# Performance work log

Hardware: AMD Instinct MI355X
Metric: run time of the kernel (lower is better)

The kernel has to match this reference:

```python
import jax, jax.numpy as jnp
import numpy as np

I, H, O = 512, 1024, 2  # input_size, hidden_size, output_size
B, S = 64, 512          # batch, seq_len


def setup_inputs() -> dict:
    key = jax.random.key(0)
    ks = jax.random.split(key, 9)
    sc = 1.0 / np.sqrt(I + H)
    return {
        "x": jax.random.normal(ks[0], (B, S, I), dtype=jnp.float32),
        "h": jnp.zeros((B, 1, H), dtype=jnp.float32),
        "Wz": jax.random.uniform(ks[1], (I + H, H), jnp.float32, -sc, sc),
        "bz": jax.random.uniform(ks[2], (H,), jnp.float32, -sc, sc),
        "Wr": jax.random.uniform(ks[3], (I + H, H), jnp.float32, -sc, sc),
        "br": jax.random.uniform(ks[4], (H,), jnp.float32, -sc, sc),
        "Wh": jax.random.uniform(ks[5], (I + H, H), jnp.float32, -sc, sc),
        "bh": jax.random.uniform(ks[6], (H,), jnp.float32, -sc, sc),
        "Wfc": jax.random.uniform(ks[7], (H, O), jnp.float32, -1.0 / np.sqrt(H), 1.0 / np.sqrt(H)),
        "bfc": jax.random.uniform(ks[8], (O,), jnp.float32, -1.0 / np.sqrt(H), 1.0 / np.sqrt(H)),
    }


def reference(x, h, Wz, bz, Wr, br, Wh, bh, Wfc, bfc):
    h0 = jnp.squeeze(h, axis=1)  # (B, H)

    def step(hid, xt):  # xt: (B, I), hid: (B, H)
        ih = jnp.concatenate([xt, hid], axis=1)              # (B, I+H)
        z = jax.nn.sigmoid(ih @ Wz + bz)                     # update gate
        r = jax.nn.sigmoid(ih @ Wr + br)                     # reset gate
        ihr = jnp.concatenate([xt, r * hid], axis=1)
        h_cand = jnp.tanh(ihr @ Wh + bh)
        new_h = (1.0 - z) * hid + z * h_cand
        return new_h, None

    x_t = jnp.transpose(x, (1, 0, 2))  # (S, B, I)
    h_last, _ = jax.lax.scan(step, h0, x_t)
    out = jax.nn.relu(h_last) @ Wfc + bfc  # (B, O)
    return jax.nn.log_softmax(out, axis=1)
```

## Files before the change

### kernel.cpp

```cpp
#include <hip/hip_runtime.h>

typedef __attribute__((ext_vector_type(4))) short bf4;
typedef __attribute__((ext_vector_type(8))) short bf8;
typedef __attribute__((ext_vector_type(4))) float f4;

#define BB 64
#define SS 512
#define II 512
#define HH 1024
#define SCH 64
#define NCH 8
#define GBLK 64

__device__ __forceinline__ short f2bf(float f) {
  unsigned u = __float_as_uint(f);
  u = u + 0x7fff + ((u >> 16) & 1);
  return (short)(u >> 16);
}
__device__ __forceinline__ float bf2f(short s) {
  return __uint_as_float(((unsigned)(unsigned short)s) << 16);
}
__device__ __forceinline__ float sigm(float x) {
  return 1.0f / (1.0f + __expf(-x));
}
__device__ __forceinline__ float tanh_f(float x) {
  float e = __expf(-2.0f * fabsf(x));
  float t = (1.0f - e) / (1.0f + e);
  return copysignf(t, x);
}

__device__ __forceinline__ unsigned long long ld_u64_l3(const unsigned long long* p) {
  return __hip_atomic_load((unsigned long long*)p, __ATOMIC_RELAXED, __HIP_MEMORY_SCOPE_AGENT);
}
__device__ __forceinline__ void st_u32_l3(unsigned* p, unsigned v) {
  __hip_atomic_store(p, v, __ATOMIC_RELAXED, __HIP_MEMORY_SCOPE_AGENT);
}


__global__ __launch_bounds__(256) void cast_x_k(const float* __restrict__ x, short* __restrict__ xb) {
  size_t i = ((size_t)blockIdx.x * 256 + threadIdx.x) * 4;
  float4 v = *(const float4*)(x + i);
  bf4 o; o[0] = f2bf(v.x); o[1] = f2bf(v.y); o[2] = f2bf(v.z); o[3] = f2bf(v.w);
  *(bf4*)(xb + i) = o;
}

__global__ __launch_bounds__(256) void prep_wxt_k(const float* __restrict__ Wz, const float* __restrict__ Wr,
                                                  const float* __restrict__ Wh, short* __restrict__ WxT) {
  int idx = blockIdx.x * 256 + threadIdx.x;
  int g = idx >> 19;
  int rem = idx & 524287;
  int n = rem >> 9, k = rem & 511;
  const float* W = (g == 0) ? Wz : (g == 1) ? Wr : Wh;
  WxT[idx] = f2bf(W[(size_t)k * HH + n]);
}

__global__ __launch_bounds__(256) void prep_uswz_k(const float* __restrict__ Wz, const float* __restrict__ Wr,
                                                   const float* __restrict__ Wh, short* __restrict__ Us) {
  int t = blockIdx.x * 256 + threadIdx.x;
  int lane = t & 63, kk = (t >> 6) & 31, nb = (t >> 11) & 63, g = t >> 17;
  const float* W = (g == 0) ? Wz : (g == 1) ? Wr : Wh;
  int n = nb * 16 + (lane & 15);
  int kb = II + kk * 32 + (lane >> 4) * 8;
  bf8 o;
#pragma unroll
  for (int j = 0; j < 8; j++) o[j] = f2bf(W[(size_t)(kb + j) * HH + n]);
  *(bf8*)(Us + (size_t)t * 8) = o;
}

__global__ __launch_bounds__(256) void init_h_k(const float* __restrict__ h, float* __restrict__ h32,
                                                short* __restrict__ hb) {
  int i = blockIdx.x * 256 + threadIdx.x;
  float v = h[i];
  h32[i] = v; hb[i] = f2bf(v);
}

__global__ __launch_bounds__(256) void gemm_k(const short* __restrict__ xb, const short* __restrict__ WxT,
                                              const float* __restrict__ bz, const float* __restrict__ br,
                                              const float* __restrict__ bh, short* __restrict__ Gx, int s0) {
  __shared__ short Al[4 * 64 * 8];
  __shared__ short Bl[4 * 64 * 8];
  int tid = threadIdx.x, wave = tid >> 6, lane = tid & 63;
  int sl = blockIdx.x;
  int n0 = blockIdx.y * 64;
  f4 acc[4] = {};
  int mp = tid >> 2, q = tid & 3;
  const short* asrc = xb + ((size_t)mp * SS + (s0 + sl)) * II + q * 8;
  int ng = n0 + mp;
  int gb = ng >> 10, hb_ = ng & 1023;
  const short* bsrc = WxT + ((size_t)gb * HH + hb_) * II + q * 8;
  int adst = ((mp >> 4) * 64 + q * 16 + (mp & 15)) * 8;

  for (int kk = 0; kk < II; kk += 32) {
    bf8 av = *(const bf8*)(asrc + kk);
    bf8 bv = *(const bf8*)(bsrc + kk);
    __syncthreads();
    *(bf8*)&Al[adst] = av;
    *(bf8*)&Bl[adst] = bv;
    __syncthreads();
    bf8 af = *(bf8*)&Al[(wave * 64 + lane) * 8];
#pragma unroll
    for (int ns = 0; ns < 4; ns++) {
      bf8 bfr = *(bf8*)&Bl[(ns * 64 + lane) * 8];
      acc[ns] = __builtin_amdgcn_mfma_f32_16x16x32_bf16(af, bfr, acc[ns], 0, 0, 0);
    }
  }
  int brow0 = wave * 16 + (lane >> 4) * 4;
#pragma unroll
  for (int ns = 0; ns < 4; ns++) {
    int ngl = n0 + ns * 16 + (lane & 15);
    int g2 = ngl >> 10, h2 = ngl & 1023;
    float bias = ((g2 == 0) ? bz : (g2 == 1) ? br : bh)[h2];
    bf4 o;
#pragma unroll
    for (int i = 0; i < 4; i++) o[i] = f2bf(acc[ns][i] + bias);
    *(bf4*)&Gx[(((size_t)sl * 3 + g2) * HH + h2) * BB + brow0] = o;
  }
}


__device__ __forceinline__ void gbar(unsigned* flags, unsigned target) {
  __syncthreads();
  if (threadIdx.x == 0)
    __hip_atomic_store(&flags[blockIdx.x], target, __ATOMIC_RELEASE, __HIP_MEMORY_SCOPE_AGENT);
  if (threadIdx.x < GBLK) {
    while (__hip_atomic_load(&flags[threadIdx.x], __ATOMIC_RELAXED, __HIP_MEMORY_SCOPE_AGENT) < target)
      __builtin_amdgcn_s_sleep(1);
  }
  __asm__ volatile("" ::: "memory");
  __syncthreads();
}

union HL { unsigned long long u[2]; bf8 v; };

__global__ __launch_bounds__(256) void rec_k(const short* __restrict__ Gx, const short* __restrict__ Us,
                                             float* __restrict__ h32, short* hb,
                                             short* rhb, unsigned* flags) {
  __shared__ short Uzr[2 * 32 * 64 * 8];
  int tid = threadIdx.x, wave = tid >> 6, lane = tid & 63, bid = blockIdx.x;
  {
    const bf8* sz = (const bf8*)Us + ((size_t)(0 * 64 + bid)) * 2048;
    const bf8* sr = (const bf8*)Us + ((size_t)(1 * 64 + bid)) * 2048;
    bf8* d = (bf8*)Uzr;
    for (int i = tid; i < 2048; i += 256) { d[i] = sz[i]; d[2048 + i] = sr[i]; }
  }
  const bf8* Uh = (const bf8*)Us + ((size_t)(2 * 64 + bid)) * 2048;

  int n0 = bid * 16;
  int brow0 = wave * 16 + (lane >> 4) * 4;
  int ncol = n0 + (lane & 15);
  float hreg[4];
#pragma unroll
  for (int i = 0; i < 4; i++) hreg[i] = h32[(size_t)(brow0 + i) * HH + ncol];
  __syncthreads();

  size_t aoff = ((size_t)(wave * 16 + (lane & 15)) * HH + (lane >> 4) * 8) / 4;
  const unsigned long long* hq  = (const unsigned long long*)hb  + aoff;
  const unsigned long long* rhq = (const unsigned long long*)rhb + aoff;

  unsigned target = 0;
  for (int t = 0; t < SCH; t++) {
    const short* gz = Gx + (((size_t)t * 3 + 0) * HH + ncol) * BB + brow0;
    bf4 gzv = *(const bf4*)gz;
    bf4 grv = *(const bf4*)(gz + (size_t)HH * BB);
    bf4 ghv = *(const bf4*)(gz + 2 * (size_t)HH * BB);
    f4 zacc = {}, racc = {};
#pragma unroll
    for (int g = 0; g < 4; g++) {
      HL a[8];
#pragma unroll
      for (int j = 0; j < 8; j++) {
        int kk = g * 8 + j;
        a[j].u[0] = ld_u64_l3(hq + kk * 8);
        a[j].u[1] = ld_u64_l3(hq + kk * 8 + 1);
      }
#pragma unroll
      for (int j = 0; j < 8; j++) {
        int kk = g * 8 + j;
        bf8 b0 = *(bf8*)&Uzr[(kk * 64 + lane) * 8];
        zacc = __builtin_amdgcn_mfma_f32_16x16x32_bf16(a[j].v, b0, zacc, 0, 0, 0);
        bf8 b1 = *(bf8*)&Uzr[(2048 + kk * 64 + lane) * 8];
        racc = __builtin_amdgcn_mfma_f32_16x16x32_bf16(a[j].v, b1, racc, 0, 0, 0);
      }
    }
    float zf[4];
#pragma unroll
    for (int i = 0; i < 4; i++) {
      zf[i] = sigm(zacc[i] + bf2f(gzv[i]));
      float r = sigm(racc[i] + bf2f(grv[i]));
      unsigned sv = (unsigned)(unsigned short)f2bf(r * hreg[i]);
      unsigned up = __shfl_down(sv, 1);
      if (!(lane & 1))
        st_u32_l3((unsigned*)rhb + ((size_t)(brow0 + i) * HH + ncol) / 2, sv | (up << 16));
    }
    gbar(flags, ++target);
    f4 cacc = {};
#pragma unroll
    for (int g = 0; g < 4; g++) {
      HL a[8];
#pragma unroll
      for (int j = 0; j < 8; j++) {
        int kk = g * 8 + j;
        a[j].u[0] = ld_u64_l3(rhq + kk * 8);
        a[j].u[1] = ld_u64_l3(rhq + kk * 8 + 1);
      }
#pragma unroll
      for (int j = 0; j < 8; j++) {
        int kk = g * 8 + j;
        bf8 b2 = Uh[kk * 64 + lane];
        cacc = __builtin_amdgcn_mfma_f32_16x16x32_bf16(a[j].v, b2, cacc, 0, 0, 0);
      }
    }
#pragma unroll
    for (int i = 0; i < 4; i++) {
      float c = tanh_f(cacc[i] + bf2f(ghv[i]));
      float hn = hreg[i] + zf[i] * (c - hreg[i]);
      hreg[i] = hn;
      unsigned sv = (unsigned)(unsigned short)f2bf(hn);
      unsigned up = __shfl_down(sv, 1);
      if (!(lane & 1))
        st_u32_l3((unsigned*)hb + ((size_t)(brow0 + i) * HH + ncol) / 2, sv | (up << 16));
    }
    gbar(flags, ++target);
  }
#pragma unroll
  for (int i = 0; i < 4; i++) h32[(size_t)(brow0 + i) * HH + ncol] = hreg[i];
}


__global__ __launch_bounds__(64) void out_k(const float* __restrict__ h32, const float* __restrict__ Wfc,
                                            const float* __restrict__ bfc, float* __restrict__ out) {
  int b = blockIdx.x, t = threadIdx.x;
  float a0 = 0.f, a1 = 0.f;
  for (int k = t; k < HH; k += 64) {
    float hv = fmaxf(h32[(size_t)b * HH + k], 0.f);
    a0 += hv * Wfc[k * 2]; a1 += hv * Wfc[k * 2 + 1];
  }
#pragma unroll
  for (int off = 32; off > 0; off >>= 1) { a0 += __shfl_down(a0, off); a1 += __shfl_down(a1, off); }
  if (t == 0) {
    float y0 = a0 + bfc[0], y1 = a1 + bfc[1];
    float m = fmaxf(y0, y1);
    float lse = m + logf(__expf(y0 - m) + __expf(y1 - m));
    out[b * 2] = y0 - lse; out[b * 2 + 1] = y1 - lse;
  }
}


extern "C" void kernel_launch(void* const* d_in, const int* in_sizes, int n_in,
                              void* d_out, int out_size, void* d_ws, size_t ws_size,
                              hipStream_t stream) {
  const float* x   = (const float*)d_in[0];
  const float* h0  = (const float*)d_in[1];
  const float* Wz  = (const float*)d_in[2];
  const float* bz  = (const float*)d_in[3];
  const float* Wr  = (const float*)d_in[4];
  const float* br  = (const float*)d_in[5];
  const float* Wh  = (const float*)d_in[6];
  const float* bh  = (const float*)d_in[7];
  const float* Wfc = (const float*)d_in[8];
  const float* bfc = (const float*)d_in[9];
  float* out = (float*)d_out;

  char* ws = (char*)d_ws;
  short*    xb    = (short*)(ws);
  short*    WxT   = (short*)(ws + 33554432);
  short*    Us    = (short*)(ws + 36700160);
  short*    Gx    = (short*)(ws + 42991616);
  float*    h32   = (float*)(ws + 68157440);
  short*    hbuf  = (short*)(ws + 68419584);
  short*    rhb   = (short*)(ws + 68550656);
  unsigned* flags = (unsigned*)(ws + 68681728);

  cast_x_k<<<16384, 256, 0, stream>>>(x, xb);
  prep_wxt_k<<<6144, 256, 0, stream>>>(Wz, Wr, Wh, WxT);
  prep_uswz_k<<<1536, 256, 0, stream>>>(Wz, Wr, Wh, Us);
  init_h_k<<<256, 256, 0, stream>>>(h0, h32, hbuf);

  for (int c = 0; c < NCH; c++) {
    gemm_k<<<dim3(SCH, 48), 256, 0, stream>>>(xb, WxT, bz, br, bh, Gx, c * SCH);
    hipMemsetAsync(flags, 0, GBLK * sizeof(unsigned), stream);
    rec_k<<<GBLK, 256, 0, stream>>>(Gx, Us, h32, hbuf, rhb, flags);
  }
  out_k<<<BB, 64, 0, stream>>>(h32, Wfc, bfc, out);
}
```

Measured before the change: 11.65 ms.

## Replace flat grid barrier with hierarchical per-XCC counter barrier

```diff
diff --git a/kernel.cpp b/kernel.cpp
--- a/kernel.cpp
+++ b/kernel.cpp
@@ -12,6 +12,11 @@
 #define NCH 8
 #define GBLK 64
 
+#define F_GINIT 0
+#define F_XCNT  32
+#define F_XARR  320
+#define F_XFLAG 608
+
 __device__ __forceinline__ short f2bf(float f) {
   unsigned u = __float_as_uint(f);
   u = u + 0x7fff + ((u >> 16) & 1);
@@ -34,6 +39,12 @@
 }
 __device__ __forceinline__ void st_u32_l3(unsigned* p, unsigned v) {
   __hip_atomic_store(p, v, __ATOMIC_RELAXED, __HIP_MEMORY_SCOPE_AGENT);
+}
+__device__ __forceinline__ unsigned rmw_read(unsigned* p) {
+  return __hip_atomic_fetch_add(p, 0u, __ATOMIC_RELAXED, __HIP_MEMORY_SCOPE_AGENT);
+}
+__device__ __forceinline__ unsigned rmw_add1(unsigned* p) {
+  return __hip_atomic_fetch_add(p, 1u, __ATOMIC_RELAXED, __HIP_MEMORY_SCOPE_AGENT);
 }
 
 
@@ -118,18 +129,6 @@
 }
 
 
-__device__ __forceinline__ void gbar(unsigned* flags, unsigned target) {
-  __syncthreads();
-  if (threadIdx.x == 0)
-    __hip_atomic_store(&flags[blockIdx.x], target, __ATOMIC_RELEASE, __HIP_MEMORY_SCOPE_AGENT);
-  if (threadIdx.x < GBLK) {
-    while (__hip_atomic_load(&flags[threadIdx.x], __ATOMIC_RELAXED, __HIP_MEMORY_SCOPE_AGENT) < target)
-      __builtin_amdgcn_s_sleep(1);
-  }
-  __asm__ volatile("" ::: "memory");
-  __syncthreads();
-}
-
 union HL { unsigned long long u[2]; bf8 v; };
 
 __global__ __launch_bounds__(256) void rec_k(const short* __restrict__ Gx, const short* __restrict__ Us,
@@ -137,6 +136,16 @@
                                              short* rhb, unsigned* flags) {
   __shared__ short Uzr[2 * 32 * 64 * 8];
   int tid = threadIdx.x, wave = tid >> 6, lane = tid & 63, bid = blockIdx.x;
+
+  unsigned myxcc;
+  __asm__ volatile("s_getreg_b32 %0, hwreg(HW_REG_XCC_ID)" : "=s"(myxcc));
+  myxcc &= 7;
+
+  if (tid == 0) {
+    rmw_add1(&flags[F_XCNT + 32 * myxcc]);
+    rmw_add1(&flags[F_GINIT]);
+  }
+
   {
     const bf8* sz = (const bf8*)Us + ((size_t)(0 * 64 + bid)) * 2048;
     const bf8* sr = (const bf8*)Us + ((size_t)(1 * 64 + bid)) * 2048;
@@ -151,6 +160,13 @@
   float hreg[4];
 #pragma unroll
   for (int i = 0; i < 4; i++) hreg[i] = h32[(size_t)(brow0 + i) * HH + ncol];
+
+  unsigned pres = 0, nown = 0;
+  if (tid < 8) {
+    while (rmw_read(&flags[F_GINIT]) < GBLK) __builtin_amdgcn_s_sleep(2);
+    pres = rmw_read(&flags[F_XCNT + 32 * tid]);
+    if (tid == 0) nown = rmw_read(&flags[F_XCNT + 32 * myxcc]);
+  }
   __syncthreads();
 
   size_t aoff = ((size_t)(wave * 16 + (lane & 15)) * HH + (lane >> 4) * 8) / 4;
@@ -192,7 +208,20 @@
       if (!(lane & 1))
         st_u32_l3((unsigned*)rhb + ((size_t)(brow0 + i) * HH + ncol) / 2, sv | (up << 16));
     }
-    gbar(flags, ++target);
+    ++target;
+    __syncthreads();
+    if (tid == 0) {
+      unsigned old = rmw_add1(&flags[F_XARR + 32 * myxcc]);
+      if (old + 1 == nown * target) {
+        __asm__ volatile("buffer_wbl2 sc1" ::: "memory");
+        __asm__ volatile("s_waitcnt vmcnt(0)" ::: "memory");
+        rmw_add1(&flags[F_XFLAG + 32 * myxcc]);
+      }
+    }
+    if (tid < 8 && pres)
+      while (rmw_read(&flags[F_XFLAG + 32 * tid]) < target) __builtin_amdgcn_s_sleep(2);
+    __asm__ volatile("" ::: "memory");
+    __syncthreads();
     f4 cacc = {};
 #pragma unroll
     for (int g = 0; g < 4; g++) {
@@ -220,7 +249,20 @@
       if (!(lane & 1))
         st_u32_l3((unsigned*)hb + ((size_t)(brow0 + i) * HH + ncol) / 2, sv | (up << 16));
     }
-    gbar(flags, ++target);
+    ++target;
+    __syncthreads();
+    if (tid == 0) {
+      unsigned old = rmw_add1(&flags[F_XARR + 32 * myxcc]);
+      if (old + 1 == nown * target) {
+        __asm__ volatile("buffer_wbl2 sc1" ::: "memory");
+        __asm__ volatile("s_waitcnt vmcnt(0)" ::: "memory");
+        rmw_add1(&flags[F_XFLAG + 32 * myxcc]);
+      }
+    }
+    if (tid < 8 && pres)
+      while (rmw_read(&flags[F_XFLAG + 32 * tid]) < target) __builtin_amdgcn_s_sleep(2);
+    __asm__ volatile("" ::: "memory");
+    __syncthreads();
   }
 #pragma unroll
   for (int i = 0; i < 4; i++) h32[(size_t)(brow0 + i) * HH + ncol] = hreg[i];
@@ -278,7 +320,7 @@
 
   for (int c = 0; c < NCH; c++) {
     gemm_k<<<dim3(SCH, 48), 256, 0, stream>>>(xb, WxT, bz, br, bh, Gx, c * SCH);
-    hipMemsetAsync(flags, 0, GBLK * sizeof(unsigned), stream);
+    hipMemsetAsync(flags, 0, 4096, stream);
     rec_k<<<GBLK, 256, 0, stream>>>(Gx, Us, h32, hbuf, rhb, flags);
   }
   out_k<<<BB, 64, 0, stream>>>(h32, Wfc, bfc, out);
```

New measurement: 10.45 ms. -10.3%, faster.
